# Kernel tuning notes

Measured on AMD Instinct MI355X. Metric: run time of the kernel, lower is better.

## Reference

```python
import jax, jax.numpy as jnp
import numpy as np

N = 100000  # nodes
E = 3200000  # edges

def setup_inputs() -> dict:
    key = jax.random.key(0)
    k1, k2, k3, k4, k5, k6 = jax.random.split(key, 6)
    x = jax.random.normal(k1, (N, 256), dtype=jnp.float32)
    adj_row = jax.random.randint(k2, (E,), 0, N, dtype=jnp.int32)
    adj_col = jax.random.randint(k3, (E,), 0, N, dtype=jnp.int32)
    adj_vals = jax.random.uniform(k4, (E,), dtype=jnp.float32)
    W = jax.random.normal(k5, (256, 256), dtype=jnp.float32) * 0.05
    b = jax.random.normal(k6, (256,), dtype=jnp.float32) * 0.05
    return {"x": x, "adj_row": adj_row, "adj_col": adj_col,
            "adj_vals": adj_vals, "W": W, "b": b}

def reference(x, adj_row, adj_col, adj_vals, W, b):
    # GCNEncoder.forward (eval mode: dropout is identity).
    # h = Linear(x): [N, D_out]
    h = jnp.dot(x, W.T) + b
    # SpMM: out[i] = sum_e adj_vals[e] * h[adj_col[e]] for edges with row i
    gathered = adj_vals[:, None] * h[adj_col]          # [E, D_out]
    out = jax.ops.segment_sum(gathered, adj_row, num_segments=N)
    return jax.nn.relu(out)
```

## Files before the change

### kernel.cpp

```cpp
#include <hip/hip_runtime.h>

#define D 256
#define BSHIFT 9
#define BROWS 512
#define MAXBK 256
#define PBLK 2048

typedef __attribute__((ext_vector_type(8))) _Float16 f16x8;
typedef __attribute__((ext_vector_type(4))) float f32x4;

#define HSCALE 5.0f

static __device__ __forceinline__ unsigned short f2h(float f) {
    _Float16 h = (_Float16)f;
    return __builtin_bit_cast(unsigned short, h);
}
static __device__ __forceinline__ int i8x(unsigned u, int sh) {
    return (int)(signed char)(u >> sh);
}

__global__ __launch_bounds__(256) void count_and_packW(
    const int* __restrict__ adj_row, int* __restrict__ blk_hist,
    const float* __restrict__ W, unsigned short* __restrict__ Wp, int E, int nbk)
{
    __shared__ int hist[MAXBK];
    const int tid = threadIdx.x;

    if (blockIdx.x < PBLK) {
        const int chunk = (E + PBLK - 1) / PBLK;
        const int e0 = blockIdx.x * chunk;
        const int e1 = min(e0 + chunk, E);

        for (int k = tid; k < nbk; k += 256) hist[k] = 0;
        __syncthreads();
        for (int i = e0 + tid; i < e1; i += 256)
            atomicAdd(&hist[adj_row[i] >> BSHIFT], 1);
        __syncthreads();
        for (int k = tid; k < nbk; k += 256)
            blk_hist[(size_t)blockIdx.x * nbk + k] = hist[k];
    } else {
        const int t = (blockIdx.x - PBLK) * 256 + tid;
        const int lane = t & 63;
        const int nt = (t >> 6) & 15;
        const int kt = t >> 10;
        const int n = nt * 16 + (lane & 15);
        const int k0 = kt * 32 + (lane >> 4) * 8;
#pragma unroll
        for (int j = 0; j < 8; ++j)
            Wp[(size_t)t * 8 + j] = f2h(W[n * D + k0 + j]);
    }
}

__global__ __launch_bounds__(256) void scan_blk_hist(
    int* __restrict__ blk_hist, int* __restrict__ cnt, int nbk)
{
    __shared__ int wsums[4];
    const int k = blockIdx.x;
    const int tid = threadIdx.x;
    const int lane = tid & 63;
    const int wid = tid >> 6;

    int vals[8];
    int tsum = 0;
#pragma unroll
    for (int j = 0; j < 8; ++j) {
        vals[j] = blk_hist[(size_t)(tid * 8 + j) * nbk + k];
        tsum += vals[j];
    }

    int v = tsum;
    for (int d = 1; d < 64; d <<= 1) {
        int u = __shfl_up(v, d, 64);
        if (lane >= d) v += u;
    }
    if (lane == 63) wsums[wid] = v;
    __syncthreads();
    int woff = 0;
    for (int w = 0; w < wid; ++w) woff += wsums[w];

    int run = woff + v - tsum;
#pragma unroll
    for (int j = 0; j < 8; ++j) {
        const int t = vals[j];
        blk_hist[(size_t)(tid * 8 + j) * nbk + k] = run;
        run += t;
    }
    if (tid == 0) cnt[k] = wsums[0] + wsums[1] + wsums[2] + wsums[3];
}

__global__ __launch_bounds__(256) void scan_cnt(
    const int* __restrict__ cnt, int* __restrict__ bbase, int nbk)
{
    __shared__ int wsums[4];
    const int tid = threadIdx.x;
    const int lane = tid & 63;
    const int wid = tid >> 6;
    const int val = (tid < nbk) ? cnt[tid] : 0;

    int v = val;
    for (int d = 1; d < 64; d <<= 1) {
        int u = __shfl_up(v, d, 64);
        if (lane >= d) v += u;
    }
    if (lane == 63) wsums[wid] = v;
    __syncthreads();
    int woff = 0;
    for (int w = 0; w < wid; ++w) woff += wsums[w];
    if (tid < nbk) bbase[tid] = woff + v - val;
}

__global__ __launch_bounds__(256) void partition_and_linear(
    const int* __restrict__ adj_row, const int* __restrict__ adj_col,
    const float* __restrict__ adj_vals, const int* __restrict__ bbase,
    const int* __restrict__ blk_hist, uint2* __restrict__ part,
    const float* __restrict__ x, const unsigned short* __restrict__ Wp,
    const float* __restrict__ b, signed char* __restrict__ hq,
    int E, int nbk, int M)
{
    __shared__ int sbase[MAXBK];
    __shared__ int lcur[MAXBK];
    const int tid = threadIdx.x;

    if (blockIdx.x < PBLK) {
        const int blk = blockIdx.x;
        const int chunk = (E + PBLK - 1) / PBLK;
        const int e0 = blk * chunk;
        const int e1 = min(e0 + chunk, E);

        for (int k = tid; k < nbk; k += 256) {
            sbase[k] = bbase[k] + blk_hist[(size_t)blk * nbk + k];
            lcur[k] = 0;
        }
        __syncthreads();

        for (int i = e0 + tid; i < e1; i += 256) {
            const int r = adj_row[i];
            const int k = r >> BSHIFT;
            const int col = __builtin_nontemporal_load(adj_col + i);
            const float val = __builtin_nontemporal_load(adj_vals + i);
            const unsigned v15 = (unsigned)(val * 32767.0f + 0.5f);
            const int pos = sbase[k] + atomicAdd(&lcur[k], 1);
            part[pos] = make_uint2(((unsigned)(r & (BROWS - 1)) << 17) | (unsigned)col, v15);
        }
        return;
    }

    const int lane = tid & 63;
    const int wave = tid >> 6;
    const int row0 = (blockIdx.x - PBLK) * 128 + wave * 32;
    const int arow = lane & 15;
    const int kgrp = lane >> 4;

    f32x4 acc[2][16];
#pragma unroll
    for (int t = 0; t < 2; ++t)
#pragma unroll
        for (int nt = 0; nt < 16; ++nt)
            acc[t][nt] = (f32x4){0.f, 0.f, 0.f, 0.f};

    for (int kt = 0; kt < 8; ++kt) {
        const int k0 = kt * 32 + kgrp * 8;
        f16x8 a[2];
#pragma unroll
        for (int t = 0; t < 2; ++t) {
            int r = row0 + t * 16 + arow;
            if (r >= M) r = M - 1;
            const f32x4* xp = (const f32x4*)(x + (size_t)r * D + k0);
            const f32x4 lo = __builtin_nontemporal_load(xp);
            const f32x4 hi = __builtin_nontemporal_load(xp + 1);
            a[t][0] = (_Float16)lo[0]; a[t][1] = (_Float16)lo[1];
            a[t][2] = (_Float16)lo[2]; a[t][3] = (_Float16)lo[3];
            a[t][4] = (_Float16)hi[0]; a[t][5] = (_Float16)hi[1];
            a[t][6] = (_Float16)hi[2]; a[t][7] = (_Float16)hi[3];
        }
        const f16x8* __restrict__ wp =
            (const f16x8*)Wp + (size_t)(kt * 16) * 64 + lane;
#pragma unroll
        for (int nt = 0; nt < 16; ++nt) {
            const f16x8 bf = wp[nt * 64];
            acc[0][nt] = __builtin_amdgcn_mfma_f32_16x16x32_f16(bf, a[0], acc[0][nt], 0, 0, 0);
            acc[1][nt] = __builtin_amdgcn_mfma_f32_16x16x32_f16(bf, a[1], acc[1][nt], 0, 0, 0);
        }
    }

    const float S = 127.0f / HSCALE;
    const int srow = lane & 15;
    const int scol0 = (lane >> 4) * 4;
#pragma unroll
    for (int t = 0; t < 2; ++t) {
        const int xrow = row0 + t * 16 + srow;
        if (xrow >= M) continue;
        signed char* hp = hq + (size_t)xrow * D;
#pragma unroll
        for (int nt = 0; nt < 16; ++nt) {
            const int wcol = nt * 16 + scol0;
            const f32x4 bv = *(const f32x4*)(b + wcol);
            unsigned pk = 0;
#pragma unroll
            for (int r = 0; r < 4; ++r) {
                const float v = fminf(fmaxf((acc[t][nt][r] + bv[r]) * S, -127.f), 127.f);
                const int q = (int)rintf(v);
                pk |= ((unsigned)q & 0xFFu) << (8 * r);
            }
            *(unsigned*)(hp + wcol) = pk;
        }
    }
}

__global__ __launch_bounds__(256) void bucket_fill(
    const uint2* __restrict__ part, const int* __restrict__ bbase,
    int* __restrict__ row_ptr, unsigned* __restrict__ csr4, int n, int E, int nbk)
{
    __shared__ int hist[BROWS];
    __shared__ int off[BROWS];
    __shared__ int wsums[4];

    const int tid = threadIdx.x;
    const int lane = tid & 63;
    const int wid = tid >> 6;
    const int bk = blockIdx.x;
    const int row0 = bk << BSHIFT;
    const int nr = min(row0 + BROWS, n) - row0;
    const int base = bbase[bk];
    const int ecnt = ((bk + 1 < nbk) ? bbase[bk + 1] : E) - base;

    for (int r = tid; r < BROWS; r += 256) hist[r] = 0;
    __syncthreads();
    for (int i = tid; i < ecnt; i += 256)
        atomicAdd(&hist[part[base + i].x >> 17], 1);
    __syncthreads();

    const int h0 = hist[2 * tid], h1 = hist[2 * tid + 1];
    const int tsum = h0 + h1;
    int v = tsum;
    for (int d = 1; d < 64; d <<= 1) {
        int u = __shfl_up(v, d, 64);
        if (lane >= d) v += u;
    }
    if (lane == 63) wsums[wid] = v;
    __syncthreads();
    int woff = 0;
    for (int w = 0; w < wid; ++w) woff += wsums[w];
    const int pref = woff + v - tsum;
    off[2 * tid] = pref;
    off[2 * tid + 1] = pref + h0;
    __syncthreads();

    for (int r = tid; r < nr; r += 256) row_ptr[row0 + r] = base + off[r];
    if (bk == nbk - 1 && tid == 0) row_ptr[n] = E;
    for (int r = tid; r < BROWS; r += 256) hist[r] = base + off[r];
    __syncthreads();

    for (int i = tid; i < ecnt; i += 256) {
        const uint2 w = part[base + i];
        const int lr = w.x >> 17;
        const int pos = atomicAdd(&hist[lr], 1);
        csr4[pos] = (w.y << 17) | (w.x & 0x1FFFF);
    }
}

__global__ __launch_bounds__(256) void gather_row(
    const int* __restrict__ row_ptr, const unsigned* __restrict__ csr4,
    const signed char* __restrict__ hq, float* __restrict__ out, int n)
{
    const int row = blockIdx.x * 4 + (threadIdx.x >> 6);
    if (row >= n) return;
    const int lane = threadIdx.x & 63;

    const int s = row_ptr[row];
    const int e = row_ptr[row + 1];

    int a0 = 0, a1 = 0, a2 = 0, a3 = 0;

    int i = s;
    for (; i + 3 < e; i += 4) {
        const unsigned w0 = csr4[i + 0];
        const unsigned w1 = csr4[i + 1];
        const unsigned w2 = csr4[i + 2];
        const unsigned w3 = csr4[i + 3];
        const unsigned d0 = ((const unsigned*)(hq + (size_t)(w0 & 0x1FFFFu) * D))[lane];
        const unsigned d1 = ((const unsigned*)(hq + (size_t)(w1 & 0x1FFFFu) * D))[lane];
        const unsigned d2 = ((const unsigned*)(hq + (size_t)(w2 & 0x1FFFFu) * D))[lane];
        const unsigned d3 = ((const unsigned*)(hq + (size_t)(w3 & 0x1FFFFu) * D))[lane];
        const int v0 = (int)(w0 >> 17);
        const int v1 = (int)(w1 >> 17);
        const int v2 = (int)(w2 >> 17);
        const int v3 = (int)(w3 >> 17);

        a0 += __mul24(v0, i8x(d0, 0))  + __mul24(v1, i8x(d1, 0))
            + __mul24(v2, i8x(d2, 0))  + __mul24(v3, i8x(d3, 0));
        a1 += __mul24(v0, i8x(d0, 8))  + __mul24(v1, i8x(d1, 8))
            + __mul24(v2, i8x(d2, 8))  + __mul24(v3, i8x(d3, 8));
        a2 += __mul24(v0, i8x(d0, 16)) + __mul24(v1, i8x(d1, 16))
            + __mul24(v2, i8x(d2, 16)) + __mul24(v3, i8x(d3, 16));
        a3 += __mul24(v0, i8x(d0, 24)) + __mul24(v1, i8x(d1, 24))
            + __mul24(v2, i8x(d2, 24)) + __mul24(v3, i8x(d3, 24));
    }
    for (; i < e; ++i) {
        const unsigned w = csr4[i];
        const unsigned d = ((const unsigned*)(hq + (size_t)(w & 0x1FFFFu) * D))[lane];
        const int v = (int)(w >> 17);
        a0 += __mul24(v, i8x(d, 0));
        a1 += __mul24(v, i8x(d, 8));
        a2 += __mul24(v, i8x(d, 16));
        a3 += __mul24(v, i8x(d, 24));
    }

    const float qs = HSCALE / (127.0f * 32767.0f);
    f32x4 st;
    st[0] = fmaxf((float)a0 * qs, 0.f); st[1] = fmaxf((float)a1 * qs, 0.f);
    st[2] = fmaxf((float)a2 * qs, 0.f); st[3] = fmaxf((float)a3 * qs, 0.f);
    *((f32x4*)(out + (size_t)row * D) + lane) = st;
}

extern "C" void kernel_launch(void* const* d_in, const int* in_sizes, int n_in,
                              void* d_out, int out_size, void* d_ws, size_t ws_size,
                              hipStream_t stream)
{
    const float* x        = (const float*)d_in[0];
    const int*   adj_row  = (const int*)d_in[1];
    const int*   adj_col  = (const int*)d_in[2];
    const float* adj_vals = (const float*)d_in[3];
    const float* W        = (const float*)d_in[4];
    const float* b        = (const float*)d_in[5];
    float*       out      = (float*)d_out;

    const int n = in_sizes[0] / D;
    const int E = in_sizes[1];
    const int nbk = (n + BROWS - 1) >> BSHIFT;

    char* ws = (char*)d_ws;
    size_t off = 0;
    auto alloc = [&](size_t bytes) {
        size_t o = off;
        off += (bytes + 255) & ~(size_t)255;
        return o;
    };
    signed char* hq    = (signed char*)(ws + alloc((size_t)n * D));
    unsigned short* Wp = (unsigned short*)(ws + alloc((size_t)8192 * 8 * sizeof(unsigned short)));
    int*      blk_hist = (int*)     (ws + alloc((size_t)PBLK * nbk * sizeof(int)));
    int*      cnt      = (int*)     (ws + alloc((size_t)MAXBK * sizeof(int)));
    int*      bbase    = (int*)     (ws + alloc((size_t)MAXBK * sizeof(int)));
    int*      row_ptr  = (int*)     (ws + alloc((size_t)(n + 1) * sizeof(int)));
    uint2*    part     = (uint2*)   (ws + alloc((size_t)E * sizeof(uint2)));
    unsigned* csr4     = (unsigned*)(ws + alloc((size_t)E * sizeof(unsigned)));
    (void)ws_size;

    count_and_packW<<<PBLK + 32, 256, 0, stream>>>(adj_row, blk_hist, W, Wp, E, nbk);

    scan_blk_hist<<<nbk, 256, 0, stream>>>(blk_hist, cnt, nbk);
    scan_cnt<<<1, 256, 0, stream>>>(cnt, bbase, nbk);

    const int linBlocks = (n + 127) / 128;
    partition_and_linear<<<PBLK + linBlocks, 256, 0, stream>>>(
        adj_row, adj_col, adj_vals, bbase, blk_hist, part, x, Wp, b, hq, E, nbk, n);

    bucket_fill<<<nbk, 256, 0, stream>>>(part, bbase, row_ptr, csr4, n, E, nbk);

    gather_row<<<(n + 3) / 4, 256, 0, stream>>>(row_ptr, csr4, hq, out, n);
}
```

Before: 301.5 us.

## Split fused partition/linear kernel into separate launches; shrink linear tile to 16 rows per wave

Un-fuses the edge partition and the MFMA linear projection, which had shared one grid, into two kernels. The linear now runs after bucket_fill as its own launch, with each wave handling 16 rows instead of 32 and x read with ordinary loads instead of nontemporal ones. This removes the co-scheduling of two very different workloads and halves per-wave accumulator registers to raise occupancy. In exchange it gives up the overlap between partitioning and GEMM, adds a launch, and each W fragment is reused across fewer rows.

```diff
diff --git a/kernel.cpp b/kernel.cpp
--- a/kernel.cpp
+++ b/kernel.cpp
@@ -109,101 +109,92 @@
     if (tid < nbk) bbase[tid] = woff + v - val;
 }
 
-__global__ __launch_bounds__(256) void partition_and_linear(
+__global__ __launch_bounds__(256) void partition_edges(
     const int* __restrict__ adj_row, const int* __restrict__ adj_col,
     const float* __restrict__ adj_vals, const int* __restrict__ bbase,
-    const int* __restrict__ blk_hist, uint2* __restrict__ part,
-    const float* __restrict__ x, const unsigned short* __restrict__ Wp,
-    const float* __restrict__ b, signed char* __restrict__ hq,
-    int E, int nbk, int M)
+    const int* __restrict__ blk_hist, uint2* __restrict__ part, int E, int nbk)
 {
     __shared__ int sbase[MAXBK];
     __shared__ int lcur[MAXBK];
     const int tid = threadIdx.x;
-
-    if (blockIdx.x < PBLK) {
-        const int blk = blockIdx.x;
-        const int chunk = (E + PBLK - 1) / PBLK;
-        const int e0 = blk * chunk;
-        const int e1 = min(e0 + chunk, E);
-
-        for (int k = tid; k < nbk; k += 256) {
-            sbase[k] = bbase[k] + blk_hist[(size_t)blk * nbk + k];
-            lcur[k] = 0;
-        }
-        __syncthreads();
-
-        for (int i = e0 + tid; i < e1; i += 256) {
-            const int r = adj_row[i];
-            const int k = r >> BSHIFT;
-            const int col = __builtin_nontemporal_load(adj_col + i);
-            const float val = __builtin_nontemporal_load(adj_vals + i);
-            const unsigned v15 = (unsigned)(val * 32767.0f + 0.5f);
-            const int pos = sbase[k] + atomicAdd(&lcur[k], 1);
-            part[pos] = make_uint2(((unsigned)(r & (BROWS - 1)) << 17) | (unsigned)col, v15);
-        }
-        return;
-    }
-
-    const int lane = tid & 63;
-    const int wave = tid >> 6;
-    const int row0 = (blockIdx.x - PBLK) * 128 + wave * 32;
+    const int blk = blockIdx.x;
+    const int chunk = (E + PBLK - 1) / PBLK;
+    const int e0 = blk * chunk;
+    const int e1 = min(e0 + chunk, E);
+
+    for (int k = tid; k < nbk; k += 256) {
+        sbase[k] = bbase[k] + blk_hist[(size_t)blk * nbk + k];
+        lcur[k] = 0;
+    }
+    __syncthreads();
+
+    for (int i = e0 + tid; i < e1; i += 256) {
+        const int r = adj_row[i];
+        const int k = r >> BSHIFT;
+        const int col = __builtin_nontemporal_load(adj_col + i);
+        const float val = __builtin_nontemporal_load(adj_vals + i);
+        const unsigned v15 = (unsigned)(val * 32767.0f + 0.5f);
+        const int pos = sbase[k] + atomicAdd(&lcur[k], 1);
+        part[pos] = make_uint2(((unsigned)(r & (BROWS - 1)) << 17) | (unsigned)col, v15);
+    }
+}
+
+__global__ __launch_bounds__(256) void mfma_linear(
+    const float* __restrict__ x, const unsigned short* __restrict__ Wp,
+    const float* __restrict__ b, signed char* __restrict__ hq, int M)
+{
+    const int lane = threadIdx.x & 63;
+    const int wave = threadIdx.x >> 6;
+    const int row0 = blockIdx.x * 64 + wave * 16;
     const int arow = lane & 15;
     const int kgrp = lane >> 4;
 
-    f32x4 acc[2][16];
-#pragma unroll
-    for (int t = 0; t < 2; ++t)
-#pragma unroll
-        for (int nt = 0; nt < 16; ++nt)
-            acc[t][nt] = (f32x4){0.f, 0.f, 0.f, 0.f};
+    f32x4 acc[16];
+#pragma unroll
+    for (int nt = 0; nt < 16; ++nt)
+        acc[nt] = (f32x4){0.f, 0.f, 0.f, 0.f};
+
+    int r = row0 + arow;
+    if (r >= M) r = M - 1;
+    const float* xrow = x + (size_t)r * D;
 
     for (int kt = 0; kt < 8; ++kt) {
         const int k0 = kt * 32 + kgrp * 8;
-        f16x8 a[2];
-#pragma unroll
-        for (int t = 0; t < 2; ++t) {
-            int r = row0 + t * 16 + arow;
-            if (r >= M) r = M - 1;
-            const f32x4* xp = (const f32x4*)(x + (size_t)r * D + k0);
-            const f32x4 lo = __builtin_nontemporal_load(xp);
-            const f32x4 hi = __builtin_nontemporal_load(xp + 1);
-            a[t][0] = (_Float16)lo[0]; a[t][1] = (_Float16)lo[1];
-            a[t][2] = (_Float16)lo[2]; a[t][3] = (_Float16)lo[3];
-            a[t][4] = (_Float16)hi[0]; a[t][5] = (_Float16)hi[1];
-            a[t][6] = (_Float16)hi[2]; a[t][7] = (_Float16)hi[3];
-        }
+        const f32x4 lo = *(const f32x4*)(xrow + k0);
+        const f32x4 hi = *(const f32x4*)(xrow + k0 + 4);
+        f16x8 a;
+        a[0] = (_Float16)lo[0]; a[1] = (_Float16)lo[1];
+        a[2] = (_Float16)lo[2]; a[3] = (_Float16)lo[3];
+        a[4] = (_Float16)hi[0]; a[5] = (_Float16)hi[1];
+        a[6] = (_Float16)hi[2]; a[7] = (_Float16)hi[3];
+
         const f16x8* __restrict__ wp =
             (const f16x8*)Wp + (size_t)(kt * 16) * 64 + lane;
 #pragma unroll
         for (int nt = 0; nt < 16; ++nt) {
             const f16x8 bf = wp[nt * 64];
-            acc[0][nt] = __builtin_amdgcn_mfma_f32_16x16x32_f16(bf, a[0], acc[0][nt], 0, 0, 0);
-            acc[1][nt] = __builtin_amdgcn_mfma_f32_16x16x32_f16(bf, a[1], acc[1][nt], 0, 0, 0);
+            acc[nt] = __builtin_amdgcn_mfma_f32_16x16x32_f16(bf, a, acc[nt], 0, 0, 0);
         }
     }
 
     const float S = 127.0f / HSCALE;
     const int srow = lane & 15;
     const int scol0 = (lane >> 4) * 4;
-#pragma unroll
-    for (int t = 0; t < 2; ++t) {
-        const int xrow = row0 + t * 16 + srow;
-        if (xrow >= M) continue;
-        signed char* hp = hq + (size_t)xrow * D;
-#pragma unroll
-        for (int nt = 0; nt < 16; ++nt) {
-            const int wcol = nt * 16 + scol0;
-            const f32x4 bv = *(const f32x4*)(b + wcol);
-            unsigned pk = 0;
-#pragma unroll
-            for (int r = 0; r < 4; ++r) {
-                const float v = fminf(fmaxf((acc[t][nt][r] + bv[r]) * S, -127.f), 127.f);
-                const int q = (int)rintf(v);
-                pk |= ((unsigned)q & 0xFFu) << (8 * r);
-            }
-            *(unsigned*)(hp + wcol) = pk;
+    const int orow = row0 + srow;
+    if (orow >= M) return;
+    signed char* hp = hq + (size_t)orow * D;
+#pragma unroll
+    for (int nt = 0; nt < 16; ++nt) {
+        const int wcol = nt * 16 + scol0;
+        const f32x4 bv = *(const f32x4*)(b + wcol);
+        unsigned pk = 0;
+#pragma unroll
+        for (int rr = 0; rr < 4; ++rr) {
+            const float v = fminf(fmaxf((acc[nt][rr] + bv[rr]) * S, -127.f), 127.f);
+            const int q = (int)rintf(v);
+            pk |= ((unsigned)q & 0xFFu) << (8 * rr);
         }
+        *(unsigned*)(hp + wcol) = pk;
     }
 }
 
@@ -351,11 +342,11 @@
     scan_blk_hist<<<nbk, 256, 0, stream>>>(blk_hist, cnt, nbk);
     scan_cnt<<<1, 256, 0, stream>>>(cnt, bbase, nbk);
 
-    const int linBlocks = (n + 127) / 128;
-    partition_and_linear<<<PBLK + linBlocks, 256, 0, stream>>>(
-        adj_row, adj_col, adj_vals, bbase, blk_hist, part, x, Wp, b, hq, E, nbk, n);
+    partition_edges<<<PBLK, 256, 0, stream>>>(adj_row, adj_col, adj_vals, bbase, blk_hist, part, E, nbk);
 
     bucket_fill<<<nbk, 256, 0, stream>>>(part, bbase, row_ptr, csr4, n, E, nbk);
 
+    mfma_linear<<<(n + 63) / 64, 256, 0, stream>>>(x, Wp, b, hq, n);
+
     gather_row<<<(n + 3) / 4, 256, 0, stream>>>(row_ptr, csr4, hq, out, n);
 }
```

New measurement: 298.6 us. Within noise of the previous version (-0.9%).
